# Kernel tuning notes

Hardware: AMD Instinct MI355X
Metric: run time of the kernel (lower is better)

Reference implementation:

```python
import jax, jax.numpy as jnp
import numpy as np

N = 50000
E = 800000
D = 128          # in_channels == hidden_channels
L = 3            # num_layers
JK = D * L       # jk 'cat' output
H2 = D // 2      # classifier hidden
C = 2            # out classes
EPS = 1e-5


def setup_inputs() -> dict:
    key = jax.random.key(0)
    ks = jax.random.split(key, 16)
    x = jax.random.normal(ks[0], (N, D), dtype=jnp.float32)
    edge_index = jax.random.randint(ks[1], (2, E), 0, N, dtype=jnp.int64)
    s = 0.05
    Wl = jax.random.normal(ks[2], (L, D, D), dtype=jnp.float32) * s   # lin_l (on aggregated), has bias
    bl = jax.random.normal(ks[3], (L, D), dtype=jnp.float32) * s
    Wr = jax.random.normal(ks[4], (L, D, D), dtype=jnp.float32) * s   # lin_r (on root), no bias
    gamma = jnp.ones((L, D), dtype=jnp.float32)
    beta = jnp.zeros((L, D), dtype=jnp.float32)
    rmean = jax.random.normal(ks[5], (L, D), dtype=jnp.float32) * s
    rvar = jax.random.uniform(ks[6], (L, D), dtype=jnp.float32, minval=0.5, maxval=1.5)
    Wc1 = jax.random.normal(ks[7], (JK, H2), dtype=jnp.float32) * s
    bc1 = jax.random.normal(ks[8], (H2,), dtype=jnp.float32) * s
    Wc2 = jax.random.normal(ks[9], (H2, C), dtype=jnp.float32) * s
    bc2 = jax.random.normal(ks[10], (C,), dtype=jnp.float32) * s
    return {"x": x, "edge_index": edge_index, "Wl": Wl, "bl": bl, "Wr": Wr,
            "gamma": gamma, "beta": beta, "rmean": rmean, "rvar": rvar,
            "Wc1": Wc1, "bc1": bc1, "Wc2": Wc2, "bc2": bc2}


def reference(x, edge_index, Wl, bl, Wr, gamma, beta, rmean, rvar, Wc1, bc1, Wc2, bc2):
    src, dst = edge_index[0], edge_index[1]
    # node in-degree (for mean aggregation), clamp to avoid div-by-zero
    deg = jax.ops.segment_sum(jnp.ones((E,), dtype=x.dtype), dst, num_segments=N)
    inv_deg = 1.0 / jnp.maximum(deg, 1.0)  # [N]

    h = x
    layer_outputs = []
    for i in range(L):
        # SAGEConv(mean): out = lin_l(mean_{j in N(i)} h_j) + lin_r(h_i)
        agg = jax.ops.segment_sum(h[src], dst, num_segments=N) * inv_deg[:, None]  # [N, D]
        h = agg @ Wl[i] + bl[i] + h @ Wr[i]
        # BatchNorm (eval: running stats), then ReLU; Dropout is identity in eval
        h = (h - rmean[i]) * jax.lax.rsqrt(rvar[i] + EPS) * gamma[i] + beta[i]
        h = jax.nn.relu(h)
        layer_outputs.append(h)

    jk = jnp.concatenate(layer_outputs, axis=-1)  # [N, L*D]
    z = jax.nn.relu(jk @ Wc1 + bc1)
    logits = z @ Wc2 + bc2  # [N, 2]
    return logits
```

## Files before the change

### kernel.cpp

```cpp
#include <hip/hip_runtime.h>
#include <hip/hip_fp16.h>
#include <cstdint>
#include <cstddef>

#define DD 128
#define JKD 384
#define EPSV 1e-5f
#define BSH 7
#define NBMAX 512
#define PCH 8192
#define PTH 1024
#define BCAP 8192

typedef __attribute__((ext_vector_type(8))) short bf16x8;
typedef __attribute__((ext_vector_type(4))) float f32x4;
#define MFMA(a, b, c) __builtin_amdgcn_mfma_f32_16x16x32_bf16(a, b, c, 0, 0, 0)

__device__ inline unsigned short f2bf_rne(float f) {
  unsigned u = __float_as_uint(f);
  unsigned r = u + 0x7fffu + ((u >> 16) & 1u);
  return (unsigned short)(r >> 16);
}

__device__ inline void split8(const float* s, bf16x8& hi, bf16x8& lo) {
#pragma unroll
  for (int j = 0; j < 8; ++j) {
    float f = s[j];
    unsigned short h = f2bf_rne(f);
    float fh = __uint_as_float((unsigned)h << 16);
    hi[j] = (short)h;
    lo[j] = (short)f2bf_rne(f - fh);
  }
}

__device__ inline void h8_to_f8(uint4 raw, float* out) {
  const __half2* hp = reinterpret_cast<const __half2*>(&raw);
#pragma unroll
  for (int j = 0; j < 4; ++j) {
    float2 f = __half22float2(hp[j]);
    out[2 * j] = f.x;
    out[2 * j + 1] = f.y;
  }
}

__global__ __launch_bounds__(PTH) void bucket_hist(const int* __restrict__ dst,
                                                   int* __restrict__ bucket_cnt, int E) {
  __shared__ int h[NBMAX];
  int t = threadIdx.x;
  for (int i = t; i < NBMAX; i += PTH) h[i] = 0;
  __syncthreads();
  int base = blockIdx.x * PCH;
#pragma unroll
  for (int it = 0; it < PCH / PTH; ++it) {
    int e = base + it * PTH + t;
    if (e < E) {
      int d = __builtin_nontemporal_load(dst + e);
      atomicAdd(&h[d >> BSH], 1);
    }
  }
  __syncthreads();
  for (int i = t; i < NBMAX; i += PTH)
    if (h[i]) atomicAdd(&bucket_cnt[i], h[i]);
}

__global__ __launch_bounds__(512) void bucket_scan(const int* __restrict__ bucket_cnt,
                                                   int* __restrict__ bucket_start,
                                                   int* __restrict__ bucket_cursor,
                                                   int* __restrict__ row_start, int N, int E) {
  __shared__ int wsum[8];
  __shared__ int wpref[8];
  int t = threadIdx.x;
  int lane = t & 63, wid = t >> 6;
  int v = bucket_cnt[t];
  int sc = v;
#pragma unroll
  for (int off = 1; off < 64; off <<= 1) {
    int u = __shfl_up(sc, off, 64);
    if (lane >= off) sc += u;
  }
  if (lane == 63) wsum[wid] = sc;
  __syncthreads();
  if (t == 0) {
    int a = 0;
#pragma unroll
    for (int w = 0; w < 8; ++w) { wpref[w] = a; a += wsum[w]; }
  }
  __syncthreads();
  int excl = wpref[wid] + sc - v;
  bucket_start[t] = excl;
  bucket_cursor[t] = excl;
  if (t == 0) row_start[N] = E;
}

__global__ __launch_bounds__(PTH) void partition_kernel(const int* __restrict__ src,
                                                        const int* __restrict__ dst,
                                                        int* bucket_cursor,
                                                        unsigned* __restrict__ packed, int E) {
  __shared__ int h[NBMAX];
  __shared__ int lofs[NBMAX];
  __shared__ int res[NBMAX];
  __shared__ int lcur[NBMAX];
  __shared__ int wsum[4];
  __shared__ int wpref[4];
  __shared__ unsigned stage[PCH];
  int t = threadIdx.x;
  int lane = t & 63;
  int base = blockIdx.x * PCH;

  for (int i = t; i < NBMAX; i += PTH) h[i] = 0;
  __syncthreads();
#pragma unroll
  for (int it = 0; it < PCH / PTH; ++it) {
    int e = base + it * PTH + t;
    if (e < E) {
      int d = __builtin_nontemporal_load(dst + e);
      atomicAdd(&h[d >> BSH], 1);
    }
  }
  __syncthreads();
  int c0 = 0, c1 = 0, s = 0, sc = 0;
  if (t < 256) {
    c0 = h[2 * t];
    c1 = h[2 * t + 1];
    s = c0 + c1;
    sc = s;
#pragma unroll
    for (int off = 1; off < 64; off <<= 1) {
      int u = __shfl_up(sc, off, 64);
      if (lane >= off) sc += u;
    }
    if (lane == 63) wsum[t >> 6] = sc;
  }
  __syncthreads();
  if (t == 0) {
    int a = 0;
#pragma unroll
    for (int w = 0; w < 4; ++w) { wpref[w] = a; a += wsum[w]; }
  }
  __syncthreads();
  if (t < 256) {
    int excl = wpref[t >> 6] + sc - s;
    lofs[2 * t] = excl;
    lofs[2 * t + 1] = excl + c0;
    lcur[2 * t] = excl;
    lcur[2 * t + 1] = excl + c0;
    if (c0 > 0) res[2 * t] = atomicAdd(&bucket_cursor[2 * t], c0);
    if (c1 > 0) res[2 * t + 1] = atomicAdd(&bucket_cursor[2 * t + 1], c1);
  }
  __syncthreads();
#pragma unroll
  for (int it = 0; it < PCH / PTH; ++it) {
    int e = base + it * PTH + t;
    if (e < E) {
      int d = __builtin_nontemporal_load(dst + e);
      int sv = __builtin_nontemporal_load(src + e);
      int pos = atomicAdd(&lcur[d >> BSH], 1);
      stage[pos] = ((unsigned)(d & ((1 << BSH) - 1)) << 16) | (unsigned)(sv & 0xffff);
    }
  }
  __syncthreads();
  int wid = t >> 6;
  for (int b = wid; b < NBMAX; b += PTH / 64) {
    int run = h[b];
    if (run == 0) continue;
    int gbase = res[b], lbase = lofs[b];
    for (int j = lane; j < run; j += 64) packed[gbase + j] = stage[lbase + j];
  }
}

__global__ __launch_bounds__(256) void csr_build(const unsigned* __restrict__ packed,
                                                 const int* __restrict__ bucket_start,
                                                 int* __restrict__ row_start,
                                                 float* __restrict__ inv_deg,
                                                 unsigned short* __restrict__ col, int N) {
  __shared__ int cntA[128];
  __shared__ int lcur[128];
  __shared__ int wsum2[2];
  __shared__ int wpref2[2];
  __shared__ unsigned short stage[BCAP];
  int t = threadIdx.x;
  int b = blockIdx.x;
  int s0 = bucket_start[b], s1 = bucket_start[b + 1];
  int cnt = s1 - s0;
  if (t < 128) cntA[t] = 0;
  __syncthreads();
  for (int i = t; i < cnt; i += 256) {
    unsigned p = packed[s0 + i];
    atomicAdd(&cntA[p >> 16], 1);
  }
  __syncthreads();
  if (t < 128) {
    int lane = t & 63, wid = t >> 6;
    int v = cntA[t];
    int sc = v;
#pragma unroll
    for (int off = 1; off < 64; off <<= 1) {
      int u = __shfl_up(sc, off, 64);
      if (lane >= off) sc += u;
    }
    if (lane == 63) wsum2[wid] = sc;
    __syncthreads();
    if (t == 0) { wpref2[0] = 0; wpref2[1] = wsum2[0]; }
    __syncthreads();
    int excl = wpref2[wid] + sc - v;
    lcur[t] = excl;
    int node = b * 128 + t;
    if (node < N) {
      row_start[node] = s0 + excl;
      inv_deg[node] = 1.0f / fmaxf((float)v, 1.0f);
    }
  } else {
    __syncthreads();
    __syncthreads();
  }
  __syncthreads();
  for (int i = t; i < cnt; i += 256) {
    unsigned p = packed[s0 + i];
    int pos = atomicAdd(&lcur[p >> 16], 1);
    unsigned short us = (unsigned short)(p & 0xffff);
    if (pos < BCAP) stage[pos] = us;
    else col[s0 + pos] = us;
  }
  __syncthreads();
  int lim = min(cnt, BCAP);
  for (int i = t; i < lim; i += 256) col[s0 + i] = stage[i];
}

__global__ __launch_bounds__(256) void prep_all(const float* __restrict__ Wl,
                                                const float* __restrict__ Wr,
                                                bf16x8* __restrict__ wf,
                                                const float* __restrict__ Wc1,
                                                bf16x8* __restrict__ wcf,
                                                const float* __restrict__ x,
                                                unsigned short* __restrict__ x16, int N) {
  int b = blockIdx.x;
  int t = threadIdx.x;
  if (b < 48) {
    int idx = b * 256 + t;
    int lane = idx & 63;
    int ksnt = (idx >> 6) & 31;
    int mat = (idx >> 11) & 1;
    int layer = idx >> 12;
    int ks = ksnt >> 3, nt = ksnt & 7;
    int nn = nt * 16 + (lane & 15);
    int k0 = ks * 32 + (lane >> 4) * 8;
    const float* W = (mat ? Wr : Wl) + (size_t)layer * DD * DD;
    float v[8];
#pragma unroll
    for (int j = 0; j < 8; ++j) v[j] = W[(size_t)(k0 + j) * DD + nn];
    bf16x8 hi, lo;
    split8(v, hi, lo);
    size_t base = (size_t)((layer * 2 + mat) * 2) * 2048 + (size_t)ksnt * 64 + lane;
    wf[base] = hi;
    wf[base + 2048] = lo;
  } else if (b < 60) {
    int idx = (b - 48) * 256 + t;
    int lane = idx & 63;
    int ksnt = idx >> 6;
    int ks = ksnt >> 2, nt = ksnt & 3;
    int nn = nt * 16 + (lane & 15);
    int k0 = ks * 32 + (lane >> 4) * 8;
    float v[8];
#pragma unroll
    for (int j = 0; j < 8; ++j) v[j] = Wc1[(size_t)(k0 + j) * 64 + nn];
    bf16x8 hi, lo;
    split8(v, hi, lo);
    wcf[idx] = hi;
    wcf[idx + 3072] = lo;
  } else {
    int idx = (b - 60) * 256 + t;
    int r = idx >> 4, cc = (idx & 15) * 8;
    if (r >= N) return;
    const float* p = x + (size_t)r * DD + cc;
    float4 a = *reinterpret_cast<const float4*>(p);
    float4 bb = *reinterpret_cast<const float4*>(p + 4);
    __half2 h0 = __floats2half2_rn(a.x, a.y);
    __half2 h1 = __floats2half2_rn(a.z, a.w);
    __half2 h2 = __floats2half2_rn(bb.x, bb.y);
    __half2 h3 = __floats2half2_rn(bb.z, bb.w);
    uint4 o;
    o.x = *reinterpret_cast<unsigned*>(&h0);
    o.y = *reinterpret_cast<unsigned*>(&h1);
    o.z = *reinterpret_cast<unsigned*>(&h2);
    o.w = *reinterpret_cast<unsigned*>(&h3);
    *reinterpret_cast<uint4*>(x16 + (size_t)r * DD + cc) = o;
  }
}

__global__ __launch_bounds__(256) void agg16_kernel(const unsigned short* __restrict__ h16,
                                                    int ldh,
                                                    const int* __restrict__ row_start,
                                                    const unsigned short* __restrict__ col,
                                                    const float* __restrict__ inv_deg,
                                                    unsigned short* __restrict__ agg16, int n) {
  int wib = threadIdx.x >> 6;
  int lane = threadIdx.x & 63;
  int node = blockIdx.x * 4 + wib;
  if (node >= n) return;
  int beg = row_start[node];
  int end = row_start[node + 1];
  int q = lane >> 4, l15 = lane & 15;
  float acc[8];
#pragma unroll
  for (int k = 0; k < 8; ++k) acc[k] = 0.f;

  for (int j0 = beg; j0 < end; j0 += 16) {
    int cnt = end - j0;
    if (cnt > 16) cnt = 16;
    int cidx = (int)col[j0 + min(l15, cnt - 1)];
    uint4 raw[4];
    bool val[4];
#pragma unroll
    for (int k = 0; k < 4; ++k) {
      int e = k * 4 + q;
      int s = __shfl(cidx, e < cnt ? e : 0);
      val[k] = e < cnt;
      if (val[k]) raw[k] = *reinterpret_cast<const uint4*>(h16 + (size_t)s * ldh + l15 * 8);
    }
#pragma unroll
    for (int k = 0; k < 4; ++k) {
      if (val[k]) {
        float f8[8];
        h8_to_f8(raw[k], f8);
#pragma unroll
        for (int c = 0; c < 8; ++c) acc[c] += f8[c];
      }
    }
  }
#pragma unroll
  for (int m = 16; m <= 32; m <<= 1) {
#pragma unroll
    for (int k = 0; k < 8; ++k) acc[k] += __shfl_xor(acc[k], m);
  }
  if (lane < 16) {
    float w = inv_deg[node];
    __half2 h0 = __floats2half2_rn(acc[0] * w, acc[1] * w);
    __half2 h1 = __floats2half2_rn(acc[2] * w, acc[3] * w);
    __half2 h2 = __floats2half2_rn(acc[4] * w, acc[5] * w);
    __half2 h3 = __floats2half2_rn(acc[6] * w, acc[7] * w);
    uint4 o;
    o.x = *reinterpret_cast<unsigned*>(&h0);
    o.y = *reinterpret_cast<unsigned*>(&h1);
    o.z = *reinterpret_cast<unsigned*>(&h2);
    o.w = *reinterpret_cast<unsigned*>(&h3);
    *reinterpret_cast<uint4*>(agg16 + (size_t)node * DD + l15 * 8) = o;
  }
}

__global__ __launch_bounds__(256) void layer_gemm_mfma(
    const unsigned short* __restrict__ hin16, int ldh,
    const unsigned short* __restrict__ agg16,
    const bf16x8* __restrict__ Blh_g, const bf16x8* __restrict__ Bll_g,
    const bf16x8* __restrict__ Brh_g, const bf16x8* __restrict__ Brl_g,
    const float* __restrict__ bl, const float* __restrict__ gamma,
    const float* __restrict__ beta, const float* __restrict__ rmean,
    const float* __restrict__ rvar, unsigned short* __restrict__ out16, int n) {
  int t = threadIdx.x;
  int w = t >> 6, lane = t & 63;
  int lane16 = lane & 15, quad = lane >> 4;
  int row0 = blockIdx.x * 64;
  int m = row0 + w * 16 + lane16;
  bool valid = m < n;
  size_t mrow = (size_t)(valid ? m : 0);
  const unsigned short* ap = agg16 + mrow * DD + quad * 8;
  const unsigned short* hp = hin16 + mrow * (size_t)ldh + quad * 8;

  bf16x8 Ah[4], Al[4], Hh[4], Hl[4];
#pragma unroll
  for (int ks = 0; ks < 4; ++ks) {
    float a8[8], h8[8];
    if (valid) {
      uint4 ra = *reinterpret_cast<const uint4*>(ap + ks * 32);
      uint4 rh = *reinterpret_cast<const uint4*>(hp + ks * 32);
      h8_to_f8(ra, a8);
      h8_to_f8(rh, h8);
    } else {
#pragma unroll
      for (int j = 0; j < 8; ++j) { a8[j] = 0.f; h8[j] = 0.f; }
    }
    split8(a8, Ah[ks], Al[ks]);
    split8(h8, Hh[ks], Hl[ks]);
  }

  f32x4 acc[8];
#pragma unroll
  for (int nt = 0; nt < 8; ++nt) acc[nt] = (f32x4){0.f, 0.f, 0.f, 0.f};

#pragma unroll
  for (int ks = 0; ks < 4; ++ks) {
    int fb = ks * 8 * 64 + lane;
    bf16x8 B0[8], B1[8];
#pragma unroll
    for (int nt = 0; nt < 8; ++nt) B0[nt] = Blh_g[fb + nt * 64];
#pragma unroll
    for (int nt = 0; nt < 8; ++nt) acc[nt] = MFMA(Ah[ks], B0[nt], acc[nt]);
#pragma unroll
    for (int nt = 0; nt < 8; ++nt) B1[nt] = Bll_g[fb + nt * 64];
#pragma unroll
    for (int nt = 0; nt < 8; ++nt) acc[nt] = MFMA(Al[ks], B0[nt], acc[nt]);
#pragma unroll
    for (int nt = 0; nt < 8; ++nt) acc[nt] = MFMA(Ah[ks], B1[nt], acc[nt]);
#pragma unroll
    for (int nt = 0; nt < 8; ++nt) B0[nt] = Brh_g[fb + nt * 64];
#pragma unroll
    for (int nt = 0; nt < 8; ++nt) acc[nt] = MFMA(Hh[ks], B0[nt], acc[nt]);
#pragma unroll
    for (int nt = 0; nt < 8; ++nt) B1[nt] = Brl_g[fb + nt * 64];
#pragma unroll
    for (int nt = 0; nt < 8; ++nt) acc[nt] = MFMA(Hl[ks], B0[nt], acc[nt]);
#pragma unroll
    for (int nt = 0; nt < 8; ++nt) acc[nt] = MFMA(Hh[ks], B1[nt], acc[nt]);
  }

#pragma unroll
  for (int nt = 0; nt < 8; ++nt) {
    int c = nt * 16 + lane16;
    float sc = gamma[c] * rsqrtf(rvar[c] + EPSV);
    float sh = (bl[c] - rmean[c]) * sc + beta[c];
#pragma unroll
    for (int r = 0; r < 4; ++r) {
      int orow = row0 + w * 16 + quad * 4 + r;
      if (orow < n) {
        float v = fmaxf(fmaf(acc[nt][r], sc, sh), 0.f);
        __half hv = __float2half_rn(v);
        out16[(size_t)orow * JKD + c] = *reinterpret_cast<unsigned short*>(&hv);
      }
    }
  }
}

__global__ __launch_bounds__(256) void classifier_mfma(
    const unsigned short* __restrict__ jk16, const bf16x8* __restrict__ Bh_g,
    const bf16x8* __restrict__ Bl_g, const float* __restrict__ bc1,
    const float* __restrict__ Wc2, const float* __restrict__ bc2,
    float* __restrict__ out, int n) {
  __shared__ float sZ[64][65];
  int t = threadIdx.x;
  int w = t >> 6, lane = t & 63;
  int lane16 = lane & 15, quad = lane >> 4;
  int row0 = blockIdx.x * 64;
  int m = row0 + w * 16 + lane16;
  bool valid = m < n;
  const unsigned short* jp = jk16 + (size_t)(valid ? m : 0) * JKD + quad * 8;

  f32x4 acc[4];
#pragma unroll
  for (int nt = 0; nt < 4; ++nt) acc[nt] = (f32x4){0.f, 0.f, 0.f, 0.f};

#pragma unroll
  for (int ks = 0; ks < 12; ++ks) {
    float a8[8];
    if (valid) {
      uint4 raw = *reinterpret_cast<const uint4*>(jp + ks * 32);
      h8_to_f8(raw, a8);
    } else {
#pragma unroll
      for (int j = 0; j < 8; ++j) a8[j] = 0.f;
    }
    bf16x8 Jh, Jl;
    split8(a8, Jh, Jl);
    int fb = ks * 4 * 64 + lane;
    bf16x8 B0[4], B1[4];
#pragma unroll
    for (int nt = 0; nt < 4; ++nt) B0[nt] = Bh_g[fb + nt * 64];
#pragma unroll
    for (int nt = 0; nt < 4; ++nt) acc[nt] = MFMA(Jh, B0[nt], acc[nt]);
#pragma unroll
    for (int nt = 0; nt < 4; ++nt) B1[nt] = Bl_g[fb + nt * 64];
#pragma unroll
    for (int nt = 0; nt < 4; ++nt) acc[nt] = MFMA(Jl, B0[nt], acc[nt]);
#pragma unroll
    for (int nt = 0; nt < 4; ++nt) acc[nt] = MFMA(Jh, B1[nt], acc[nt]);
  }

#pragma unroll
  for (int nt = 0; nt < 4; ++nt) {
    int c = nt * 16 + lane16;
    float b1 = bc1[c];
#pragma unroll
    for (int r = 0; r < 4; ++r)
      sZ[w * 16 + quad * 4 + r][c] = fmaxf(acc[nt][r] + b1, 0.f);
  }
  __syncthreads();

  if (t < 128) {
    int r = t >> 1, j = t & 1;
    int gr = row0 + r;
    if (gr < n) {
      float s = bc2[j];
#pragma unroll
      for (int c = 0; c < 64; ++c) s = fmaf(sZ[r][c], Wc2[c * 2 + j], s);
      out[(size_t)gr * 2 + j] = s;
    }
  }
}


extern "C" void kernel_launch(void* const* d_in, const int* in_sizes, int n_in,
                              void* d_out, int out_size, void* d_ws, size_t ws_size,
                              hipStream_t stream) {
  const float* x = (const float*)d_in[0];
  const int* ei = (const int*)d_in[1];
  const float* Wl = (const float*)d_in[2];
  const float* bl = (const float*)d_in[3];
  const float* Wr = (const float*)d_in[4];
  const float* gamma = (const float*)d_in[5];
  const float* beta = (const float*)d_in[6];
  const float* rmean = (const float*)d_in[7];
  const float* rvar = (const float*)d_in[8];
  const float* Wc1 = (const float*)d_in[9];
  const float* bc1 = (const float*)d_in[10];
  const float* Wc2 = (const float*)d_in[11];
  const float* bc2 = (const float*)d_in[12];
  float* out = (float*)d_out;

  const int N = in_sizes[0] / DD;
  const int E = in_sizes[1] / 2;
  const int* src = ei;
  const int* dst = ei + E;

  auto align = [](size_t v) { return (v + 255) & ~(size_t)255; };
  char* ws = (char*)d_ws;
  size_t off = 0;
  int* row_start = (int*)(ws + off);  off = align(off + sizeof(int) * (size_t)(N + 1));
  unsigned short* col = (unsigned short*)(ws + off); off = align(off + sizeof(short) * (size_t)E);
  float* inv_deg = (float*)(ws + off); off = align(off + sizeof(float) * (size_t)N);
  unsigned* packed = (unsigned*)(ws + off); off = align(off + sizeof(unsigned) * (size_t)E);
  int* bucket_cnt = (int*)(ws + off);    off = align(off + sizeof(int) * NBMAX);
  int* bucket_start = (int*)(ws + off);  off = align(off + sizeof(int) * (NBMAX + 1));
  int* bucket_cursor = (int*)(ws + off); off = align(off + sizeof(int) * NBMAX);
  unsigned short* x16 = (unsigned short*)(ws + off);   off = align(off + sizeof(short) * (size_t)N * DD);
  unsigned short* agg16 = (unsigned short*)(ws + off); off = align(off + sizeof(short) * (size_t)N * DD);
  unsigned short* jk16 = (unsigned short*)(ws + off);  off = align(off + sizeof(short) * (size_t)N * JKD);
  bf16x8* wf = (bf16x8*)(ws + off);  off = align(off + (size_t)16 * 3 * 2 * 2 * 2048);
  bf16x8* wcf = (bf16x8*)(ws + off); off = align(off + (size_t)16 * 2 * 3072);

  const int nbuck = (N + 127) >> BSH;
  const int nChunks = (E + PCH - 1) / PCH;

  hipMemsetAsync(bucket_cnt, 0, sizeof(int) * NBMAX, stream);
  bucket_hist<<<nChunks, PTH, 0, stream>>>(dst, bucket_cnt, E);
  bucket_scan<<<1, 512, 0, stream>>>(bucket_cnt, bucket_start, bucket_cursor, row_start, N, E);
  partition_kernel<<<nChunks, PTH, 0, stream>>>(src, dst, bucket_cursor, packed, E);
  csr_build<<<nbuck, 256, 0, stream>>>(packed, bucket_start, row_start, inv_deg, col, N);

  int f16blocks = (N * 16 + 255) / 256;
  prep_all<<<60 + f16blocks, 256, 0, stream>>>(Wl, Wr, wf, Wc1, wcf, x, x16, N);

  int nTiles = (N + 63) / 64;
  for (int i = 0; i < 3; ++i) {
    const unsigned short* gsrc = (i == 0) ? x16 : (jk16 + (size_t)(i - 1) * DD);
    int ldg = (i == 0) ? DD : JKD;
    agg16_kernel<<<(N + 3) / 4, 256, 0, stream>>>(gsrc, ldg, row_start, col, inv_deg, agg16, N);
    bf16x8* Wlf = wf + (size_t)(i * 2 + 0) * 2 * 2048;
    bf16x8* Wrf = wf + (size_t)(i * 2 + 1) * 2 * 2048;
    layer_gemm_mfma<<<nTiles, 256, 0, stream>>>(
        gsrc, ldg, agg16, Wlf, Wlf + 2048, Wrf, Wrf + 2048,
        bl + (size_t)i * DD, gamma + (size_t)i * DD, beta + (size_t)i * DD,
        rmean + (size_t)i * DD, rvar + (size_t)i * DD, jk16 + (size_t)i * DD, N);
  }
  classifier_mfma<<<nTiles, 256, 0, stream>>>(jk16, wcf, wcf + 3072, bc1, Wc2, bc2, out, N);
}
```

Baseline: 315.4 us.

## Fuse last layer GEMM with classifier and merge prep into partition kernel

Per-chunk histograms are now written to global memory and summed in the scan kernel, which removes the memset and the global atomics. The weight and feature prep work is folded into the partition kernel as extra blocks, saving one launch and letting it overlap with partitioning. The third layer's GEMM is fused with the classifier, so layer-3 output stays in shared memory instead of round-tripping through jk16, which removes another launch. In exchange the scan reads about 100 chunk rows serially per thread, and the fused kernel uses more registers and shared memory, which may lower occupancy.

```diff
diff --git a/kernel.cpp b/kernel.cpp
--- a/kernel.cpp
+++ b/kernel.cpp
@@ -44,7 +44,7 @@
 }
 
 __global__ __launch_bounds__(PTH) void bucket_hist(const int* __restrict__ dst,
-                                                   int* __restrict__ bucket_cnt, int E) {
+                                                   int* __restrict__ hist_g, int E) {
   __shared__ int h[NBMAX];
   int t = threadIdx.x;
   for (int i = t; i < NBMAX; i += PTH) h[i] = 0;
@@ -59,11 +59,10 @@
     }
   }
   __syncthreads();
-  for (int i = t; i < NBMAX; i += PTH)
-    if (h[i]) atomicAdd(&bucket_cnt[i], h[i]);
-}
-
-__global__ __launch_bounds__(512) void bucket_scan(const int* __restrict__ bucket_cnt,
+  for (int i = t; i < NBMAX; i += PTH) hist_g[blockIdx.x * NBMAX + i] = h[i];
+}
+
+__global__ __launch_bounds__(512) void bucket_scan(const int* __restrict__ hist_g, int nChunks,
                                                    int* __restrict__ bucket_start,
                                                    int* __restrict__ bucket_cursor,
                                                    int* __restrict__ row_start, int N, int E) {
@@ -71,7 +70,8 @@
   __shared__ int wpref[8];
   int t = threadIdx.x;
   int lane = t & 63, wid = t >> 6;
-  int v = bucket_cnt[t];
+  int v = 0;
+  for (int c = 0; c < nChunks; ++c) v += hist_g[c * NBMAX + t];
   int sc = v;
 #pragma unroll
   for (int off = 1; off < 64; off <<= 1) {
@@ -92,10 +92,12 @@
   if (t == 0) row_start[N] = E;
 }
 
-__global__ __launch_bounds__(PTH) void partition_kernel(const int* __restrict__ src,
-                                                        const int* __restrict__ dst,
-                                                        int* bucket_cursor,
-                                                        unsigned* __restrict__ packed, int E) {
+__global__ __launch_bounds__(PTH) void partition_prep(
+    const int* __restrict__ src, const int* __restrict__ dst, int* bucket_cursor,
+    unsigned* __restrict__ packed, int E, int nChunks,
+    const float* __restrict__ Wl, const float* __restrict__ Wr, bf16x8* __restrict__ wf,
+    const float* __restrict__ Wc1, bf16x8* __restrict__ wcf,
+    const float* __restrict__ x, unsigned short* __restrict__ x16, int N) {
   __shared__ int h[NBMAX];
   __shared__ int lofs[NBMAX];
   __shared__ int res[NBMAX];
@@ -103,68 +105,127 @@
   __shared__ int wsum[4];
   __shared__ int wpref[4];
   __shared__ unsigned stage[PCH];
-  int t = threadIdx.x;
-  int lane = t & 63;
-  int base = blockIdx.x * PCH;
-
-  for (int i = t; i < NBMAX; i += PTH) h[i] = 0;
-  __syncthreads();
-#pragma unroll
-  for (int it = 0; it < PCH / PTH; ++it) {
-    int e = base + it * PTH + t;
-    if (e < E) {
-      int d = __builtin_nontemporal_load(dst + e);
-      atomicAdd(&h[d >> BSH], 1);
-    }
-  }
-  __syncthreads();
-  int c0 = 0, c1 = 0, s = 0, sc = 0;
-  if (t < 256) {
-    c0 = h[2 * t];
-    c1 = h[2 * t + 1];
-    s = c0 + c1;
-    sc = s;
-#pragma unroll
-    for (int off = 1; off < 64; off <<= 1) {
-      int u = __shfl_up(sc, off, 64);
-      if (lane >= off) sc += u;
-    }
-    if (lane == 63) wsum[t >> 6] = sc;
-  }
-  __syncthreads();
-  if (t == 0) {
-    int a = 0;
-#pragma unroll
-    for (int w = 0; w < 4; ++w) { wpref[w] = a; a += wsum[w]; }
-  }
-  __syncthreads();
-  if (t < 256) {
-    int excl = wpref[t >> 6] + sc - s;
-    lofs[2 * t] = excl;
-    lofs[2 * t + 1] = excl + c0;
-    lcur[2 * t] = excl;
-    lcur[2 * t + 1] = excl + c0;
-    if (c0 > 0) res[2 * t] = atomicAdd(&bucket_cursor[2 * t], c0);
-    if (c1 > 0) res[2 * t + 1] = atomicAdd(&bucket_cursor[2 * t + 1], c1);
-  }
-  __syncthreads();
-#pragma unroll
-  for (int it = 0; it < PCH / PTH; ++it) {
-    int e = base + it * PTH + t;
-    if (e < E) {
-      int d = __builtin_nontemporal_load(dst + e);
-      int sv = __builtin_nontemporal_load(src + e);
-      int pos = atomicAdd(&lcur[d >> BSH], 1);
-      stage[pos] = ((unsigned)(d & ((1 << BSH) - 1)) << 16) | (unsigned)(sv & 0xffff);
-    }
-  }
-  __syncthreads();
-  int wid = t >> 6;
-  for (int b = wid; b < NBMAX; b += PTH / 64) {
-    int run = h[b];
-    if (run == 0) continue;
-    int gbase = res[b], lbase = lofs[b];
-    for (int j = lane; j < run; j += 64) packed[gbase + j] = stage[lbase + j];
+
+  if (blockIdx.x < nChunks) {
+    int t = threadIdx.x;
+    int lane = t & 63;
+    int base = blockIdx.x * PCH;
+    for (int i = t; i < NBMAX; i += PTH) h[i] = 0;
+    __syncthreads();
+#pragma unroll
+    for (int it = 0; it < PCH / PTH; ++it) {
+      int e = base + it * PTH + t;
+      if (e < E) {
+        int d = __builtin_nontemporal_load(dst + e);
+        atomicAdd(&h[d >> BSH], 1);
+      }
+    }
+    __syncthreads();
+    int c0 = 0, c1 = 0, s = 0, sc = 0;
+    if (t < 256) {
+      c0 = h[2 * t];
+      c1 = h[2 * t + 1];
+      s = c0 + c1;
+      sc = s;
+#pragma unroll
+      for (int off = 1; off < 64; off <<= 1) {
+        int u = __shfl_up(sc, off, 64);
+        if (lane >= off) sc += u;
+      }
+      if (lane == 63) wsum[t >> 6] = sc;
+    }
+    __syncthreads();
+    if (t == 0) {
+      int a = 0;
+#pragma unroll
+      for (int w = 0; w < 4; ++w) { wpref[w] = a; a += wsum[w]; }
+    }
+    __syncthreads();
+    if (t < 256) {
+      int excl = wpref[t >> 6] + sc - s;
+      lofs[2 * t] = excl;
+      lofs[2 * t + 1] = excl + c0;
+      lcur[2 * t] = excl;
+      lcur[2 * t + 1] = excl + c0;
+      if (c0 > 0) res[2 * t] = atomicAdd(&bucket_cursor[2 * t], c0);
+      if (c1 > 0) res[2 * t + 1] = atomicAdd(&bucket_cursor[2 * t + 1], c1);
+    }
+    __syncthreads();
+#pragma unroll
+    for (int it = 0; it < PCH / PTH; ++it) {
+      int e = base + it * PTH + t;
+      if (e < E) {
+        int d = __builtin_nontemporal_load(dst + e);
+        int sv = __builtin_nontemporal_load(src + e);
+        int pos = atomicAdd(&lcur[d >> BSH], 1);
+        stage[pos] = ((unsigned)(d & ((1 << BSH) - 1)) << 16) | (unsigned)(sv & 0xffff);
+      }
+    }
+    __syncthreads();
+    int wid = t >> 6;
+    for (int b = wid; b < NBMAX; b += PTH / 64) {
+      int run = h[b];
+      if (run == 0) continue;
+      int gbase = res[b], lbase = lofs[b];
+      for (int j = lane; j < run; j += 64) packed[gbase + j] = stage[lbase + j];
+    }
+  } else {
+    int sub = threadIdx.x >> 8;
+    int t = threadIdx.x & 255;
+    int f16blocks = (N * 16 + 255) / 256;
+    int vb = (blockIdx.x - nChunks) * 4 + sub;
+    if (vb >= 60 + f16blocks) return;
+    if (vb < 48) {
+      int idx = vb * 256 + t;
+      int ln = idx & 63;
+      int ksnt = (idx >> 6) & 31;
+      int mat = (idx >> 11) & 1;
+      int layer = idx >> 12;
+      int ks = ksnt >> 3, nt = ksnt & 7;
+      int nn = nt * 16 + (ln & 15);
+      int k0 = ks * 32 + (ln >> 4) * 8;
+      const float* W = (mat ? Wr : Wl) + (size_t)layer * DD * DD;
+      float v[8];
+#pragma unroll
+      for (int j = 0; j < 8; ++j) v[j] = W[(size_t)(k0 + j) * DD + nn];
+      bf16x8 hi, lo;
+      split8(v, hi, lo);
+      size_t base = (size_t)((layer * 2 + mat) * 2) * 2048 + (size_t)ksnt * 64 + ln;
+      wf[base] = hi;
+      wf[base + 2048] = lo;
+    } else if (vb < 60) {
+      int idx = (vb - 48) * 256 + t;
+      int ln = idx & 63;
+      int ksnt = idx >> 6;
+      int ks = ksnt >> 2, nt = ksnt & 3;
+      int nn = nt * 16 + (ln & 15);
+      int k0 = ks * 32 + (ln >> 4) * 8;
+      float v[8];
+#pragma unroll
+      for (int j = 0; j < 8; ++j) v[j] = Wc1[(size_t)(k0 + j) * 64 + nn];
+      bf16x8 hi, lo;
+      split8(v, hi, lo);
+      wcf[idx] = hi;
+      wcf[idx + 3072] = lo;
+    } else {
+      int idx = (vb - 60) * 256 + t;
+      int r = idx >> 4, cc = (idx & 15) * 8;
+      if (r < N) {
+        const float* p = x + (size_t)r * DD + cc;
+        float4 a = *reinterpret_cast<const float4*>(p);
+        float4 bb = *reinterpret_cast<const float4*>(p + 4);
+        __half2 h0 = __floats2half2_rn(a.x, a.y);
+        __half2 h1 = __floats2half2_rn(a.z, a.w);
+        __half2 h2 = __floats2half2_rn(bb.x, bb.y);
+        __half2 h3 = __floats2half2_rn(bb.z, bb.w);
+        uint4 o;
+        o.x = *reinterpret_cast<unsigned*>(&h0);
+        o.y = *reinterpret_cast<unsigned*>(&h1);
+        o.z = *reinterpret_cast<unsigned*>(&h2);
+        o.w = *reinterpret_cast<unsigned*>(&h3);
+        *reinterpret_cast<uint4*>(x16 + (size_t)r * DD + cc) = o;
+      }
+    }
   }
 }
 
@@ -224,67 +285,6 @@
   __syncthreads();
   int lim = min(cnt, BCAP);
   for (int i = t; i < lim; i += 256) col[s0 + i] = stage[i];
-}
-
-__global__ __launch_bounds__(256) void prep_all(const float* __restrict__ Wl,
-                                                const float* __restrict__ Wr,
-                                                bf16x8* __restrict__ wf,
-                                                const float* __restrict__ Wc1,
-                                                bf16x8* __restrict__ wcf,
-                                                const float* __restrict__ x,
-                                                unsigned short* __restrict__ x16, int N) {
-  int b = blockIdx.x;
-  int t = threadIdx.x;
-  if (b < 48) {
-    int idx = b * 256 + t;
-    int lane = idx & 63;
-    int ksnt = (idx >> 6) & 31;
-    int mat = (idx >> 11) & 1;
-    int layer = idx >> 12;
-    int ks = ksnt >> 3, nt = ksnt & 7;
-    int nn = nt * 16 + (lane & 15);
-    int k0 = ks * 32 + (lane >> 4) * 8;
-    const float* W = (mat ? Wr : Wl) + (size_t)layer * DD * DD;
-    float v[8];
-#pragma unroll
-    for (int j = 0; j < 8; ++j) v[j] = W[(size_t)(k0 + j) * DD + nn];
-    bf16x8 hi, lo;
-    split8(v, hi, lo);
-    size_t base = (size_t)((layer * 2 + mat) * 2) * 2048 + (size_t)ksnt * 64 + lane;
-    wf[base] = hi;
-    wf[base + 2048] = lo;
-  } else if (b < 60) {
-    int idx = (b - 48) * 256 + t;
-    int lane = idx & 63;
-    int ksnt = idx >> 6;
-    int ks = ksnt >> 2, nt = ksnt & 3;
-    int nn = nt * 16 + (lane & 15);
-    int k0 = ks * 32 + (lane >> 4) * 8;
-    float v[8];
-#pragma unroll
-    for (int j = 0; j < 8; ++j) v[j] = Wc1[(size_t)(k0 + j) * 64 + nn];
-    bf16x8 hi, lo;
-    split8(v, hi, lo);
-    wcf[idx] = hi;
-    wcf[idx + 3072] = lo;
-  } else {
-    int idx = (b - 60) * 256 + t;
-    int r = idx >> 4, cc = (idx & 15) * 8;
-    if (r >= N) return;
-    const float* p = x + (size_t)r * DD + cc;
-    float4 a = *reinterpret_cast<const float4*>(p);
-    float4 bb = *reinterpret_cast<const float4*>(p + 4);
-    __half2 h0 = __floats2half2_rn(a.x, a.y);
-    __half2 h1 = __floats2half2_rn(a.z, a.w);
-    __half2 h2 = __floats2half2_rn(bb.x, bb.y);
-    __half2 h3 = __floats2half2_rn(bb.z, bb.w);
-    uint4 o;
-    o.x = *reinterpret_cast<unsigned*>(&h0);
-    o.y = *reinterpret_cast<unsigned*>(&h1);
-    o.z = *reinterpret_cast<unsigned*>(&h2);
-    o.w = *reinterpret_cast<unsigned*>(&h3);
-    *reinterpret_cast<uint4*>(x16 + (size_t)r * DD + cc) = o;
-  }
 }
 
 __global__ __launch_bounds__(256) void agg16_kernel(const unsigned short* __restrict__ h16,
@@ -429,11 +429,18 @@
   }
 }
 
-__global__ __launch_bounds__(256) void classifier_mfma(
-    const unsigned short* __restrict__ jk16, const bf16x8* __restrict__ Bh_g,
-    const bf16x8* __restrict__ Bl_g, const float* __restrict__ bc1,
-    const float* __restrict__ Wc2, const float* __restrict__ bc2,
-    float* __restrict__ out, int n) {
+__global__ __launch_bounds__(256) void gemm2_cls(
+    const unsigned short* __restrict__ gsrc, int ldg,
+    const unsigned short* __restrict__ agg16,
+    const bf16x8* __restrict__ Blh_g, const bf16x8* __restrict__ Bll_g,
+    const bf16x8* __restrict__ Brh_g, const bf16x8* __restrict__ Brl_g,
+    const float* __restrict__ bl, const float* __restrict__ gamma,
+    const float* __restrict__ beta, const float* __restrict__ rmean,
+    const float* __restrict__ rvar,
+    const unsigned short* __restrict__ jk16, const bf16x8* __restrict__ wcf,
+    const float* __restrict__ bc1, const float* __restrict__ Wc2,
+    const float* __restrict__ bc2, float* __restrict__ out, int n) {
+  __shared__ unsigned short sOut[4][16][136];
   __shared__ float sZ[64][65];
   int t = threadIdx.x;
   int w = t >> 6, lane = t & 63;
@@ -441,36 +448,105 @@
   int row0 = blockIdx.x * 64;
   int m = row0 + w * 16 + lane16;
   bool valid = m < n;
-  const unsigned short* jp = jk16 + (size_t)(valid ? m : 0) * JKD + quad * 8;
-
-  f32x4 acc[4];
-#pragma unroll
-  for (int nt = 0; nt < 4; ++nt) acc[nt] = (f32x4){0.f, 0.f, 0.f, 0.f};
+  size_t mrow = (size_t)(valid ? m : 0);
+  const unsigned short* ap = agg16 + mrow * DD + quad * 8;
+  const unsigned short* hp = gsrc + mrow * (size_t)ldg + quad * 8;
+
+  bf16x8 Ah[4], Al[4], Hh[4], Hl[4];
+#pragma unroll
+  for (int ks = 0; ks < 4; ++ks) {
+    float a8[8], h8[8];
+    if (valid) {
+      uint4 ra = *reinterpret_cast<const uint4*>(ap + ks * 32);
+      uint4 rh = *reinterpret_cast<const uint4*>(hp + ks * 32);
+      h8_to_f8(ra, a8);
+      h8_to_f8(rh, h8);
+    } else {
+#pragma unroll
+      for (int j = 0; j < 8; ++j) { a8[j] = 0.f; h8[j] = 0.f; }
+    }
+    split8(a8, Ah[ks], Al[ks]);
+    split8(h8, Hh[ks], Hl[ks]);
+  }
+
+  f32x4 acc[8];
+#pragma unroll
+  for (int nt = 0; nt < 8; ++nt) acc[nt] = (f32x4){0.f, 0.f, 0.f, 0.f};
+
+#pragma unroll
+  for (int ks = 0; ks < 4; ++ks) {
+    int fb = ks * 8 * 64 + lane;
+    bf16x8 B0[8], B1[8];
+#pragma unroll
+    for (int nt = 0; nt < 8; ++nt) B0[nt] = Blh_g[fb + nt * 64];
+#pragma unroll
+    for (int nt = 0; nt < 8; ++nt) acc[nt] = MFMA(Ah[ks], B0[nt], acc[nt]);
+#pragma unroll
+    for (int nt = 0; nt < 8; ++nt) B1[nt] = Bll_g[fb + nt * 64];
+#pragma unroll
+    for (int nt = 0; nt < 8; ++nt) acc[nt] = MFMA(Al[ks], B0[nt], acc[nt]);
+#pragma unroll
+    for (int nt = 0; nt < 8; ++nt) acc[nt] = MFMA(Ah[ks], B1[nt], acc[nt]);
+#pragma unroll
+    for (int nt = 0; nt < 8; ++nt) B0[nt] = Brh_g[fb + nt * 64];
+#pragma unroll
+    for (int nt = 0; nt < 8; ++nt) acc[nt] = MFMA(Hh[ks], B0[nt], acc[nt]);
+#pragma unroll
+    for (int nt = 0; nt < 8; ++nt) B1[nt] = Brl_g[fb + nt * 64];
+#pragma unroll
+    for (int nt = 0; nt < 8; ++nt) acc[nt] = MFMA(Hl[ks], B0[nt], acc[nt]);
+#pragma unroll
+    for (int nt = 0; nt < 8; ++nt) acc[nt] = MFMA(Hh[ks], B1[nt], acc[nt]);
+  }
+
+#pragma unroll
+  for (int nt = 0; nt < 8; ++nt) {
+    int c = nt * 16 + lane16;
+    float sc = gamma[c] * rsqrtf(rvar[c] + EPSV);
+    float sh = (bl[c] - rmean[c]) * sc + beta[c];
+#pragma unroll
+    for (int r = 0; r < 4; ++r) {
+      float v = fmaxf(fmaf(acc[nt][r], sc, sh), 0.f);
+      __half hv = __float2half_rn(v);
+      sOut[w][quad * 4 + r][c] = *reinterpret_cast<unsigned short*>(&hv);
+    }
+  }
+  __syncthreads();
+
+  const unsigned short* jp = jk16 + mrow * JKD + quad * 8;
+  f32x4 cacc[4];
+#pragma unroll
+  for (int nt = 0; nt < 4; ++nt) cacc[nt] = (f32x4){0.f, 0.f, 0.f, 0.f};
 
 #pragma unroll
   for (int ks = 0; ks < 12; ++ks) {
     float a8[8];
-    if (valid) {
-      uint4 raw = *reinterpret_cast<const uint4*>(jp + ks * 32);
+    if (ks < 8) {
+      if (valid) {
+        uint4 raw = *reinterpret_cast<const uint4*>(jp + ks * 32);
+        h8_to_f8(raw, a8);
+      } else {
+#pragma unroll
+        for (int j = 0; j < 8; ++j) a8[j] = 0.f;
+      }
+    } else {
+      uint4 raw = *reinterpret_cast<const uint4*>(&sOut[w][lane16][(ks - 8) * 32 + quad * 8]);
       h8_to_f8(raw, a8);
-    } else {
-#pragma unroll
-      for (int j = 0; j < 8; ++j) a8[j] = 0.f;
     }
     bf16x8 Jh, Jl;
     split8(a8, Jh, Jl);
     int fb = ks * 4 * 64 + lane;
     bf16x8 B0[4], B1[4];
 #pragma unroll
-    for (int nt = 0; nt < 4; ++nt) B0[nt] = Bh_g[fb + nt * 64];
-#pragma unroll
-    for (int nt = 0; nt < 4; ++nt) acc[nt] = MFMA(Jh, B0[nt], acc[nt]);
-#pragma unroll
-    for (int nt = 0; nt < 4; ++nt) B1[nt] = Bl_g[fb + nt * 64];
-#pragma unroll
-    for (int nt = 0; nt < 4; ++nt) acc[nt] = MFMA(Jl, B0[nt], acc[nt]);
-#pragma unroll
-    for (int nt = 0; nt < 4; ++nt) acc[nt] = MFMA(Jh, B1[nt], acc[nt]);
+    for (int nt = 0; nt < 4; ++nt) B0[nt] = wcf[fb + nt * 64];
+#pragma unroll
+    for (int nt = 0; nt < 4; ++nt) cacc[nt] = MFMA(Jh, B0[nt], cacc[nt]);
+#pragma unroll
+    for (int nt = 0; nt < 4; ++nt) B1[nt] = wcf[3072 + fb + nt * 64];
+#pragma unroll
+    for (int nt = 0; nt < 4; ++nt) cacc[nt] = MFMA(Jl, B0[nt], cacc[nt]);
+#pragma unroll
+    for (int nt = 0; nt < 4; ++nt) cacc[nt] = MFMA(Jh, B1[nt], cacc[nt]);
   }
 
 #pragma unroll
@@ -479,7 +555,7 @@
     float b1 = bc1[c];
 #pragma unroll
     for (int r = 0; r < 4; ++r)
-      sZ[w * 16 + quad * 4 + r][c] = fmaxf(acc[nt][r] + b1, 0.f);
+      sZ[w * 16 + quad * 4 + r][c] = fmaxf(cacc[nt][r] + b1, 0.f);
   }
   __syncthreads();
 
@@ -526,7 +602,8 @@
   unsigned short* col = (unsigned short*)(ws + off); off = align(off + sizeof(short) * (size_t)E);
   float* inv_deg = (float*)(ws + off); off = align(off + sizeof(float) * (size_t)N);
   unsigned* packed = (unsigned*)(ws + off); off = align(off + sizeof(unsigned) * (size_t)E);
-  int* bucket_cnt = (int*)(ws + off);    off = align(off + sizeof(int) * NBMAX);
+  const int nChunks = (E + PCH - 1) / PCH;
+  int* hist_g = (int*)(ws + off);        off = align(off + sizeof(int) * (size_t)nChunks * NBMAX);
   int* bucket_start = (int*)(ws + off);  off = align(off + sizeof(int) * (NBMAX + 1));
   int* bucket_cursor = (int*)(ws + off); off = align(off + sizeof(int) * NBMAX);
   unsigned short* x16 = (unsigned short*)(ws + off);   off = align(off + sizeof(short) * (size_t)N * DD);
@@ -536,16 +613,14 @@
   bf16x8* wcf = (bf16x8*)(ws + off); off = align(off + (size_t)16 * 2 * 3072);
 
   const int nbuck = (N + 127) >> BSH;
-  const int nChunks = (E + PCH - 1) / PCH;
-
-  hipMemsetAsync(bucket_cnt, 0, sizeof(int) * NBMAX, stream);
-  bucket_hist<<<nChunks, PTH, 0, stream>>>(dst, bucket_cnt, E);
-  bucket_scan<<<1, 512, 0, stream>>>(bucket_cnt, bucket_start, bucket_cursor, row_start, N, E);
-  partition_kernel<<<nChunks, PTH, 0, stream>>>(src, dst, bucket_cursor, packed, E);
+  int f16blocks = (N * 16 + 255) / 256;
+  int prepBlocks = (60 + f16blocks + 3) / 4;
+
+  bucket_hist<<<nChunks, PTH, 0, stream>>>(dst, hist_g, E);
+  bucket_scan<<<1, 512, 0, stream>>>(hist_g, nChunks, bucket_start, bucket_cursor, row_start, N, E);
+  partition_prep<<<nChunks + prepBlocks, PTH, 0, stream>>>(
+      src, dst, bucket_cursor, packed, E, nChunks, Wl, Wr, wf, Wc1, wcf, x, x16, N);
   csr_build<<<nbuck, 256, 0, stream>>>(packed, bucket_start, row_start, inv_deg, col, N);
-
-  int f16blocks = (N * 16 + 255) / 256;
-  prep_all<<<60 + f16blocks, 256, 0, stream>>>(Wl, Wr, wf, Wc1, wcf, x, x16, N);
 
   int nTiles = (N + 63) / 64;
   for (int i = 0; i < 3; ++i) {
@@ -554,10 +629,17 @@
     agg16_kernel<<<(N + 3) / 4, 256, 0, stream>>>(gsrc, ldg, row_start, col, inv_deg, agg16, N);
     bf16x8* Wlf = wf + (size_t)(i * 2 + 0) * 2 * 2048;
     bf16x8* Wrf = wf + (size_t)(i * 2 + 1) * 2 * 2048;
-    layer_gemm_mfma<<<nTiles, 256, 0, stream>>>(
-        gsrc, ldg, agg16, Wlf, Wlf + 2048, Wrf, Wrf + 2048,
-        bl + (size_t)i * DD, gamma + (size_t)i * DD, beta + (size_t)i * DD,
-        rmean + (size_t)i * DD, rvar + (size_t)i * DD, jk16 + (size_t)i * DD, N);
-  }
-  classifier_mfma<<<nTiles, 256, 0, stream>>>(jk16, wcf, wcf + 3072, bc1, Wc2, bc2, out, N);
-}
+    if (i < 2) {
+      layer_gemm_mfma<<<nTiles, 256, 0, stream>>>(
+          gsrc, ldg, agg16, Wlf, Wlf + 2048, Wrf, Wrf + 2048,
+          bl + (size_t)i * DD, gamma + (size_t)i * DD, beta + (size_t)i * DD,
+          rmean + (size_t)i * DD, rvar + (size_t)i * DD, jk16 + (size_t)i * DD, N);
+    } else {
+      gemm2_cls<<<nTiles, 256, 0, stream>>>(
+          gsrc, ldg, agg16, Wlf, Wlf + 2048, Wrf, Wrf + 2048,
+          bl + (size_t)i * DD, gamma + (size_t)i * DD, beta + (size_t)i * DD,
+          rmean + (size_t)i * DD, rvar + (size_t)i * DD,
+          jk16, wcf, bc1, Wc2, bc2, out, N);
+    }
+  }
+}
```

Result: no change. 315.0 us (-0.1%).
